# Kernel optimization log

Measured on AMD Instinct MI355X. Metric: run time of the kernel, lower is better.

The kernel has to match this reference:

```python
import jax, jax.numpy as jnp
import numpy as np

N_HEAD, D_K = 16, 64  # from init_kwargs (d_v == d_k)

def setup_inputs() -> dict:
    key = jax.random.key(0)
    ks = jax.random.split(key, 8)
    B, S, D, DFF = 8, 1024, 1024, 4096
    s = 1.0 / np.sqrt(D)
    return {
        "enc_input": jax.random.normal(ks[0], (B, S, D), jnp.float32),
        "mask": jnp.ones((B, 1, S), jnp.int32),
        "gap": 1,
        "wq": jax.random.normal(ks[1], (D, N_HEAD * D_K), jnp.float32) * s,
        "wk": jax.random.normal(ks[2], (D, N_HEAD * D_K), jnp.float32) * s,
        "wv": jax.random.normal(ks[3], (D, N_HEAD * D_K), jnp.float32) * s,
        "wo": jax.random.normal(ks[4], (N_HEAD * D_K, D), jnp.float32) * s,
        "w1": jax.random.normal(ks[5], (D, DFF), jnp.float32) * s,
        "b1": jnp.zeros((DFF,), jnp.float32),
        "w2": jax.random.normal(ks[6], (DFF, D), jnp.float32) * (1.0 / np.sqrt(DFF)),
        "b2": jnp.zeros((D,), jnp.float32),
    }

def reference(enc_input, mask, gap, wq, wk, wv, wo, w1, b1, w2, b2):
    # dropout=0, use_layer_norm=0, adapter=0 are hard-coded in EncoderLayer.__init__
    B, S, D = enc_input.shape
    H, dk = N_HEAD, D_K
    temperature = dk ** 0.5

    q = (enc_input @ wq).reshape(B, S, H, dk).transpose(0, 2, 1, 3)  # [B,H,S,dk]
    k = (enc_input @ wk).reshape(B, S, H, dk).transpose(0, 2, 1, 3)
    v = (enc_input @ wv).reshape(B, S, H, dk).transpose(0, 2, 1, 3)

    attn = jnp.einsum('bhqd,bhkd->bhqk', q / temperature, k)  # [B,H,S,S]
    # mask [B,1,S] -> unsqueeze head dim -> [B,1,1,S]
    attn = jnp.where(mask[:, None] == 0, jnp.float32(-1e9), attn)
    attn = jax.nn.softmax(attn, axis=-1)

    ctx = jnp.einsum('bhqk,bhkd->bhqd', attn, v)          # [B,H,S,dk]
    ctx = ctx.transpose(0, 2, 1, 3).reshape(B, S, H * dk)  # [B,S,D]
    enc = ctx @ wo + enc_input                              # attn residual

    ffn = jax.nn.relu(enc @ w1 + b1) @ w2 + b2
    out = ffn + enc                                         # ffn residual
    return out, attn
```

## Files before the change

kernel.cpp:

```cpp
#include <hip/hip_runtime.h>
#include <hip/hip_bf16.h>
#include <stdint.h>

typedef __bf16 bf16x8 __attribute__((ext_vector_type(8)));
typedef float  f32x4  __attribute__((ext_vector_type(4)));

typedef __attribute__((address_space(1))) void gvoid;
typedef __attribute__((address_space(3))) void lvoid;

__device__ __forceinline__ void async16(void* lds, const void* g) {
    __builtin_amdgcn_global_load_lds((gvoid*)g, (lvoid*)lds, 16, 0, 0);
}

__global__ void cvt_f32_to_bf16(const float* __restrict__ in,
                                __hip_bfloat16* __restrict__ out, long n) {
    long i = ((long)blockIdx.x * blockDim.x + threadIdx.x) * 4;
    if (i < n) {
        float4 v = *(const float4*)(in + i);
        __hip_bfloat162* d = (__hip_bfloat162*)(out + i);
        d[0] = __float22bfloat162_rn(make_float2(v.x, v.y));
        d[1] = __float22bfloat162_rn(make_float2(v.z, v.w));
    }
}

__global__ void transpose_f32_bf16(const float* __restrict__ in,
                                   __hip_bfloat16* __restrict__ out,
                                   int R, int C) {
    __shared__ float t[32][33];
    int c0 = blockIdx.x * 32, r0 = blockIdx.y * 32;
    int tx = threadIdx.x, ty = threadIdx.y;
#pragma unroll
    for (int i = 0; i < 4; ++i) {
        int r = r0 + ty + i * 8;
        t[ty + i * 8][tx] = in[(long)r * C + c0 + tx];
    }
    __syncthreads();
#pragma unroll
    for (int i = 0; i < 4; ++i) {
        int c = c0 + ty + i * 8;
        out[(long)c * R + r0 + tx] = __float2bfloat16(t[tx][ty + i * 8]);
    }
}

__global__ void transpose_v(const __hip_bfloat16* __restrict__ QKV,
                            __hip_bfloat16* __restrict__ Vt) {
    __shared__ __hip_bfloat16 t[32][33];
    int s0 = blockIdx.x * 32, d0 = blockIdx.y * 32, z = blockIdx.z;
    int b = z >> 4, h = z & 15;
    int tx = threadIdx.x, ty = threadIdx.y;
#pragma unroll
    for (int i = 0; i < 4; ++i) {
        int s = s0 + ty + i * 8;
        t[ty + i * 8][tx] = QKV[((long)b * 1024 + s) * 3072 + 2048 + h * 64 + d0 + tx];
    }
    __syncthreads();
#pragma unroll
    for (int i = 0; i < 4; ++i) {
        int d = d0 + ty + i * 8;
        Vt[((long)z * 64 + d) * 1024 + s0 + tx] = t[tx][ty + i * 8];
    }
}

__global__ void __launch_bounds__(256, 2)
attn_fused(const __hip_bfloat16* __restrict__ QKV,
           const __hip_bfloat16* __restrict__ Vt,
           const int* __restrict__ mask,
           float* __restrict__ attn,
           __hip_bfloat16* __restrict__ Ctx) {
    __shared__ __align__(16) __hip_bfloat16 sK[128 * 64];
    __shared__ __align__(16) __hip_bfloat16 sV[64 * 128];
    __shared__ __align__(16) __hip_bfloat16 sP[128 * 128];
    __shared__ float smadd[1024];

    const int tid = threadIdx.x, lane = tid & 63, wave = tid >> 6;
    const int r16 = lane & 15, kg = lane >> 4;

    const int dd = blockIdx.x;
    const int wgt = (dd & 7) * 128 + (dd >> 3);
    const int xblk = wgt & 7, z = wgt >> 3;
    const int b = z >> 4, h = z & 15;
    const int row0 = xblk * 128;
    const int wrow = wave * 32;

    const __hip_bfloat16* Qz = QKV + ((long)b * 1024 + row0) * 3072 + h * 64;
    const __hip_bfloat16* Kz = QKV + (long)b * 1024 * 3072 + 1024 + h * 64;
    const __hip_bfloat16* Vz = Vt + (long)z * 64 * 1024;
    float* attnZ = attn + (long)z * 1024 * 1024 + (long)row0 * 1024;

    for (int i = tid; i < 1024; i += 256)
        smadd[i] = mask[b * 1024 + i] ? 0.f : -1e9f;

    bf16x8 qa[2][2];
#pragma unroll
    for (int m = 0; m < 2; ++m)
#pragma unroll
        for (int kf = 0; kf < 2; ++kf)
            qa[m][kf] = *(const bf16x8*)(Qz + (long)(wrow + m * 16 + r16) * 3072 + kf * 32 + kg * 8);

    float mrow[2][4], lrow[2][4];
#pragma unroll
    for (int m = 0; m < 2; ++m)
#pragma unroll
        for (int i = 0; i < 4; ++i) { mrow[m][i] = -3e38f; lrow[m][i] = 0.f; }

    __syncthreads();

    const int ssw = (r16 & 7) << 4;

    for (int ct = 0; ct < 8; ++ct) {
#pragma unroll
        for (int j = 0; j < 4; ++j) {
            int c = wave * 4 + j;
            int s = c * 8 + (lane >> 3);
            int cb = (lane & 7) * 16;
            async16((char*)sK + c * 1024,
                    (const char*)(Kz + (long)(ct * 128 + s) * 3072) + (cb ^ ((s & 7) << 4)));
        }
        __syncthreads();

        f32x4 sacc[2][8];
#pragma unroll
        for (int m = 0; m < 2; ++m)
#pragma unroll
            for (int nf = 0; nf < 8; ++nf) sacc[m][nf] = f32x4{0.f, 0.f, 0.f, 0.f};

#pragma unroll
        for (int nf = 0; nf < 8; ++nf) {
            const char* kr = (const char*)sK + (nf * 16 + r16) * 128;
            bf16x8 bv0 = *(const bf16x8*)(kr + ((kg * 16) ^ ssw));
            bf16x8 bv1 = *(const bf16x8*)(kr + ((64 + kg * 16) ^ ssw));
#pragma unroll
            for (int m = 0; m < 2; ++m) {
                sacc[m][nf] = __builtin_amdgcn_mfma_f32_16x16x32_bf16(qa[m][0], bv0, sacc[m][nf], 0, 0, 0);
                sacc[m][nf] = __builtin_amdgcn_mfma_f32_16x16x32_bf16(qa[m][1], bv1, sacc[m][nf], 0, 0, 0);
            }
        }

        float madd[8];
#pragma unroll
        for (int nf = 0; nf < 8; ++nf) madd[nf] = smadd[ct * 128 + nf * 16 + r16];

#pragma unroll
        for (int m = 0; m < 2; ++m)
#pragma unroll
            for (int i = 0; i < 4; ++i) {
                float v[8];
                float tmax = -3e38f;
#pragma unroll
                for (int nf = 0; nf < 8; ++nf) {
                    float a = sacc[m][nf][i] * 0.125f + madd[nf];
                    v[nf] = a;
                    tmax = fmaxf(tmax, a);
                }
#pragma unroll
                for (int o = 1; o < 16; o <<= 1) tmax = fmaxf(tmax, __shfl_xor(tmax, o));
                float mnew = fmaxf(mrow[m][i], tmax);
                float corr = __expf(mrow[m][i] - mnew);
                float ts = 0.f;
#pragma unroll
                for (int nf = 0; nf < 8; ++nf) ts += __expf(v[nf] - mnew);
#pragma unroll
                for (int o = 1; o < 16; o <<= 1) ts += __shfl_xor(ts, o);
                lrow[m][i] = lrow[m][i] * corr + ts;
                mrow[m][i] = mnew;
            }
        __syncthreads();
    }

    float rinv[2][4];
#pragma unroll
    for (int m = 0; m < 2; ++m)
#pragma unroll
        for (int i = 0; i < 4; ++i) rinv[m][i] = 1.0f / lrow[m][i];

    f32x4 oacc[2][4];
#pragma unroll
    for (int m = 0; m < 2; ++m)
#pragma unroll
        for (int nf = 0; nf < 4; ++nf) oacc[m][nf] = f32x4{0.f, 0.f, 0.f, 0.f};

    for (int ct = 0; ct < 8; ++ct) {
#pragma unroll
        for (int j = 0; j < 4; ++j) {
            int c = wave * 4 + j;
            {
                int s = c * 8 + (lane >> 3);
                int cb = (lane & 7) * 16;
                async16((char*)sK + c * 1024,
                        (const char*)(Kz + (long)(ct * 128 + s) * 3072) + (cb ^ ((s & 7) << 4)));
            }
            {
                int dv = c * 4 + (lane >> 4);
                int cb = (lane & 15) * 16;
                async16((char*)sV + c * 1024,
                        (const char*)(Vz + (long)dv * 1024 + ct * 128) + (cb ^ ((dv & 7) << 4)));
            }
        }
        __syncthreads();

        f32x4 sacc[2][8];
#pragma unroll
        for (int m = 0; m < 2; ++m)
#pragma unroll
            for (int nf = 0; nf < 8; ++nf) sacc[m][nf] = f32x4{0.f, 0.f, 0.f, 0.f};

#pragma unroll
        for (int nf = 0; nf < 8; ++nf) {
            const char* kr = (const char*)sK + (nf * 16 + r16) * 128;
            bf16x8 bv0 = *(const bf16x8*)(kr + ((kg * 16) ^ ssw));
            bf16x8 bv1 = *(const bf16x8*)(kr + ((64 + kg * 16) ^ ssw));
#pragma unroll
            for (int m = 0; m < 2; ++m) {
                sacc[m][nf] = __builtin_amdgcn_mfma_f32_16x16x32_bf16(qa[m][0], bv0, sacc[m][nf], 0, 0, 0);
                sacc[m][nf] = __builtin_amdgcn_mfma_f32_16x16x32_bf16(qa[m][1], bv1, sacc[m][nf], 0, 0, 0);
            }
        }

        float madd[8];
#pragma unroll
        for (int nf = 0; nf < 8; ++nf) madd[nf] = smadd[ct * 128 + nf * 16 + r16];

#pragma unroll
        for (int m = 0; m < 2; ++m)
#pragma unroll
            for (int nf = 0; nf < 8; ++nf) {
                int scol = nf * 16 + r16;
#pragma unroll
                for (int i = 0; i < 4; ++i) {
                    int q = wrow + m * 16 + kg * 4 + i;
                    float p = __expf(sacc[m][nf][i] * 0.125f + madd[nf] - mrow[m][i]) * rinv[m][i];
                    attnZ[(long)q * 1024 + ct * 128 + scol] = p;
                    *(__hip_bfloat16*)((char*)sP + q * 256 + ((scol * 2) ^ ((q & 7) << 4))) =
                        __float2bfloat16(p);
                }
            }

#pragma unroll
        for (int ks = 0; ks < 4; ++ks) {
            bf16x8 pa[2], vv[4];
#pragma unroll
            for (int m = 0; m < 2; ++m)
                pa[m] = *(const bf16x8*)((const char*)sP + (wrow + m * 16 + r16) * 256 +
                                         ((ks * 64 + kg * 16) ^ ssw));
#pragma unroll
            for (int nf = 0; nf < 4; ++nf)
                vv[nf] = *(const bf16x8*)((const char*)sV + (nf * 16 + r16) * 256 +
                                          ((ks * 64 + kg * 16) ^ ssw));
#pragma unroll
            for (int m = 0; m < 2; ++m)
#pragma unroll
                for (int nf = 0; nf < 4; ++nf)
                    oacc[m][nf] = __builtin_amdgcn_mfma_f32_16x16x32_bf16(pa[m], vv[nf], oacc[m][nf], 0, 0, 0);
        }
        __syncthreads();
    }

#pragma unroll
    for (int m = 0; m < 2; ++m)
#pragma unroll
        for (int nf = 0; nf < 4; ++nf)
#pragma unroll
            for (int i = 0; i < 4; ++i) {
                int q = wrow + m * 16 + kg * 4 + i;
                Ctx[((long)b * 1024 + row0 + q) * 1024 + h * 64 + nf * 16 + r16] =
                    __float2bfloat16(oacc[m][nf][i]);
            }
}

template <int BM, int BN>
__global__ void __launch_bounds__(256)
gemm_bt(const __hip_bfloat16* __restrict__ Ab_, int lda,
        const __hip_bfloat16* __restrict__ Bt, int ldb,
        int K, float scale,
        const float* __restrict__ bias,
        const float* __restrict__ res, int ldres,
        float* __restrict__ Cf, __hip_bfloat16* __restrict__ Cb,
        int ldc, int relu) {
    constexpr int FM = BM / 32, FN = BN / 32;
    __shared__ __align__(16) __hip_bfloat16 sA[BM * 32];
    __shared__ __align__(16) __hip_bfloat16 sB[BN * 32];

    const int tid = threadIdx.x;
    const int lane = tid & 63, wave = tid >> 6;
    const int wr = wave >> 1, wc = wave & 1;
    const int r16 = lane & 15, kg = lane >> 4;
    const long row0 = (long)blockIdx.x * BM;
    const long col0 = (long)blockIdx.y * BN;

    const __hip_bfloat16* Ab = Ab_;
    const __hip_bfloat16* Bb = Bt;

    f32x4 acc[FM][FN] = {};

    for (int kt = 0; kt < K; kt += 32) {
        {
            constexpr int CHA = BM / 16;
            for (int c = wave; c < CHA; c += 4) {
                int e = c * 512 + lane * 8;
                int r = e >> 5, kk = e & 31;
                async16(&sA[c * 512], Ab + (row0 + r) * (long)lda + kt + kk);
            }
        }
        {
            constexpr int CHB = BN / 16;
            for (int c = wave; c < CHB; c += 4) {
                int e = c * 512 + lane * 8;
                int r = e >> 5, kk = e & 31;
                async16(&sB[c * 512], Bb + (col0 + r) * (long)ldb + kt + kk);
            }
        }
        __syncthreads();

        bf16x8 av[FM], bv[FN];
#pragma unroll
        for (int m = 0; m < FM; ++m)
            av[m] = *(const bf16x8*)&sA[(wr * (BM / 2) + m * 16 + r16) * 32 + kg * 8];
#pragma unroll
        for (int n = 0; n < FN; ++n)
            bv[n] = *(const bf16x8*)&sB[(wc * (BN / 2) + n * 16 + r16) * 32 + kg * 8];
#pragma unroll
        for (int m = 0; m < FM; ++m)
#pragma unroll
            for (int n = 0; n < FN; ++n)
                acc[m][n] = __builtin_amdgcn_mfma_f32_16x16x32_bf16(av[m], bv[n], acc[m][n], 0, 0, 0);
        __syncthreads();
    }

#pragma unroll
    for (int m = 0; m < FM; ++m) {
        const long rg0 = row0 + wr * (BM / 2) + m * 16 + kg * 4;
#pragma unroll
        for (int n = 0; n < FN; ++n) {
            const long cg = col0 + wc * (BN / 2) + n * 16 + r16;
#pragma unroll
            for (int i = 0; i < 4; ++i) {
                const long rg = rg0 + i;
                float v = acc[m][n][i] * scale;
                if (bias) v += bias[cg];
                if (relu) v = fmaxf(v, 0.f);
                if (res) v += res[rg * (long)ldres + cg];
                const long off = rg * (long)ldc + cg;
                if (Cf) Cf[off] = v;
                if (Cb) Cb[off] = __float2bfloat16(v);
            }
        }
    }
}

#define RDA(BUF, PM, ML, KS) \
    (*(const bf16x8*)(aRd + (BUF)*32768 + (PM)*16384 + (ML)*2048 + ((((KS)*64) + kg*16) ^ sw)))
#define RDB(BUF, PN, NL, KS) \
    (*(const bf16x8*)(bRd + (BUF)*32768 + (PN)*16384 + (NL)*2048 + ((((KS)*64) + kg*16) ^ sw)))
#define LOAD_A(BUF, PM)                          \
    _Pragma("unroll") for (int ml = 0; ml < 4; ++ml) \
    _Pragma("unroll") for (int ks = 0; ks < 2; ++ks) \
        a[ml][ks] = RDA(BUF, PM, ml, ks)
#define LOAD_B(DST, BUF, PN)                     \
    _Pragma("unroll") for (int nl = 0; nl < 2; ++nl) \
    _Pragma("unroll") for (int ks = 0; ks < 2; ++ks) \
        DST[nl][ks] = RDB(BUF, PN, nl, ks)
#define MFMA16(PM, PN, BB)                                                   \
    __builtin_amdgcn_s_setprio(1);                                           \
    _Pragma("unroll") for (int ks = 0; ks < 2; ++ks)                         \
    _Pragma("unroll") for (int ml = 0; ml < 4; ++ml)                         \
    _Pragma("unroll") for (int nl = 0; nl < 2; ++nl)                         \
        acc[(PM)*4 + ml][(PN)*2 + nl] = __builtin_amdgcn_mfma_f32_16x16x32_bf16( \
            a[ml][ks], BB[nl][ks], acc[(PM)*4 + ml][(PN)*2 + nl], 0, 0, 0);  \
    __builtin_amdgcn_s_setprio(0)
#define BAR asm volatile("s_barrier" ::: "memory")

__global__ void __launch_bounds__(512, 2)
gemm256(const __hip_bfloat16* __restrict__ A, int lda,
        const __hip_bfloat16* __restrict__ Bt, int ldb,
        int K, int Mtiles,
        const float* __restrict__ bias, int relu,
        __hip_bfloat16* __restrict__ C, int ldc) {
    __shared__ __align__(16) char lds[131072];
    const int NT = K >> 6;
    const int tid = threadIdx.x, lane = tid & 63, wave = tid >> 6;
    const int r16 = lane & 15, kg = lane >> 4;
    const int wr = wave >> 2, wc = wave & 3;
    const int sw = (r16 & 7) << 4;

    const int nwg = gridDim.x;
    const int q8 = nwg >> 3, r8 = nwg & 7;
    const int xcd = blockIdx.x & 7, rest = blockIdx.x >> 3;
    const int wg = (xcd < r8 ? xcd * (q8 + 1) : r8 * (q8 + 1) + (xcd - r8) * q8) + rest;
    const int tm = wg % Mtiles, tn = wg / Mtiles;
    const long row0 = (long)tm * 256, col0 = (long)tn * 256;

    const int idx = tid >> 3;
    const int slotp = ((tid & 7) ^ (idx & 7)) * 8;
    const __hip_bfloat16* aSrc[4];
    const __hip_bfloat16* bSrc[4];
#pragma unroll
    for (int j = 0; j < 4; ++j) {
        long ar = row0 + (j & 1) * 128 + (j >> 1) * 64 + idx;
        aSrc[j] = A + ar * lda + slotp;
        long br = col0 + ((j & 1) * 2 + (tid >> 8)) * 64 + (j >> 1) * 32 + (idx & 31);
        bSrc[j] = Bt + br * ldb + slotp;
    }

    char* ldsA = lds;
    char* ldsB = lds + 65536;
    const int stDst = wave * 1024;
    auto stA = [&](int v, int j) {
        async16(ldsA + ((v & 1) << 15) + (j << 13) + stDst, aSrc[j] + (v << 6));
    };
    auto stB = [&](int v, int j) {
        async16(ldsB + ((v & 1) << 15) + (j << 13) + stDst, bSrc[j] + (v << 6));
    };

    stA(0, 0); stA(0, 1); stB(0, 0); stB(0, 1);
    stA(0, 2); stA(0, 3); stB(0, 2); stB(0, 3);
    stA(1, 0); stA(1, 1); stB(1, 0); stB(1, 1);
    asm volatile("s_waitcnt vmcnt(4)" ::: "memory");
    BAR;

    f32x4 acc[8][4] = {};
    const char* aRd = ldsA + wr * 8192 + r16 * 128;
    const char* bRd = ldsB + wc * 4096 + r16 * 128;

    for (int u = 0; u < NT; u += 2) {
        const bool more = (u + 2) < NT;
        bf16x8 a[4][2], b0[2][2], b1[2][2];

        LOAD_A(0, 0);
        LOAD_B(b0, 0, 0);
        stA(u + 1, 2); stA(u + 1, 3);
        MFMA16(0, 0, b0);
        BAR;
        LOAD_B(b1, 0, 1);
        stB(u + 1, 2); stB(u + 1, 3);
        MFMA16(0, 1, b1);
        BAR;
        LOAD_A(0, 1);
        if (more) { stA(u + 2, 0); stA(u + 2, 1); }
        MFMA16(1, 0, b0);
        BAR;
        if (more) {
            stB(u + 2, 0); stB(u + 2, 1);
            asm volatile("s_waitcnt vmcnt(4)" ::: "memory");
        } else {
            asm volatile("s_waitcnt vmcnt(0)" ::: "memory");
        }
        MFMA16(1, 1, b1);
        BAR;
        LOAD_A(1, 0);
        LOAD_B(b0, 1, 0);
        if (more) { stA(u + 2, 2); stA(u + 2, 3); }
        MFMA16(0, 0, b0);
        BAR;
        LOAD_B(b1, 1, 1);
        if (more) { stB(u + 2, 2); stB(u + 2, 3); }
        MFMA16(0, 1, b1);
        BAR;
        LOAD_A(1, 1);
        if (more) { stA(u + 3, 0); stA(u + 3, 1); }
        MFMA16(1, 0, b0);
        BAR;
        if (more) {
            stB(u + 3, 0); stB(u + 3, 1);
            asm volatile("s_waitcnt vmcnt(4)" ::: "memory");
        }
        MFMA16(1, 1, b1);
        BAR;
    }

    const long crow = row0 + wr * 128, ccol = col0 + wc * 64;
#pragma unroll
    for (int mf = 0; mf < 8; ++mf)
#pragma unroll
        for (int nf = 0; nf < 4; ++nf) {
            const long col = ccol + nf * 16 + r16;
            const float bs = bias ? bias[col] : 0.f;
#pragma unroll
            for (int i = 0; i < 4; ++i) {
                const long row = crow + mf * 16 + kg * 4 + i;
                float v = acc[mf][nf][i] + bs;
                if (relu) v = fmaxf(v, 0.f);
                C[row * (long)ldc + col] = __float2bfloat16(v);
            }
        }
}

extern "C" void kernel_launch(void* const* d_in, const int* in_sizes, int n_in,
                              void* d_out, int out_size, void* d_ws, size_t ws_size,
                              hipStream_t stream) {
    const int B = 8, S = 1024, D = 1024, DFF = 4096;
    const long SD = (long)B * S * D;

    const float* X  = (const float*)d_in[0];
    const int*  msk = (const int*)d_in[1];
    const float* wq = (const float*)d_in[3];
    const float* wk = (const float*)d_in[4];
    const float* wv = (const float*)d_in[5];
    const float* wo = (const float*)d_in[6];
    const float* w1 = (const float*)d_in[7];
    const float* b1 = (const float*)d_in[8];
    const float* w2 = (const float*)d_in[9];
    const float* b2 = (const float*)d_in[10];

    float* out  = (float*)d_out;
    float* attn = out + SD;

    char* ws = (char*)d_ws;
    auto alloc = [&](size_t bytes) {
        char* p = ws;
        ws += (bytes + 255) & ~(size_t)255;
        return p;
    };
    __hip_bfloat16* Xb   = (__hip_bfloat16*)alloc(SD * 2);
    __hip_bfloat16* QKVb = (__hip_bfloat16*)alloc(SD * 3 * 2);
    __hip_bfloat16* Vt   = (__hip_bfloat16*)alloc(SD * 2);
    __hip_bfloat16* Ctx  = (__hip_bfloat16*)alloc(SD * 2);
    __hip_bfloat16* EncB = (__hip_bfloat16*)alloc(SD * 2);
    __hip_bfloat16* Hb   = (__hip_bfloat16*)alloc((long)B * S * DFF * 2);
    float*          EncF = (float*)alloc(SD * 4);
    __hip_bfloat16* Wcat = (__hip_bfloat16*)alloc((long)3 * D * D * 2);
    __hip_bfloat16* Wot  = (__hip_bfloat16*)alloc((long)D * D * 2);
    __hip_bfloat16* W1t  = (__hip_bfloat16*)alloc((long)D * DFF * 2);
    __hip_bfloat16* W2t  = (__hip_bfloat16*)alloc((long)D * DFF * 2);
    (void)ws_size; (void)in_sizes; (void)n_in; (void)out_size;

    dim3 tb(32, 8);
    cvt_f32_to_bf16<<<(int)(SD / 4 / 256), 256, 0, stream>>>(X, Xb, SD);
    transpose_f32_bf16<<<dim3(32, 32), tb, 0, stream>>>(wq, Wcat, D, D);
    transpose_f32_bf16<<<dim3(32, 32), tb, 0, stream>>>(wk, Wcat + (long)D * D, D, D);
    transpose_f32_bf16<<<dim3(32, 32), tb, 0, stream>>>(wv, Wcat + (long)2 * D * D, D, D);
    transpose_f32_bf16<<<dim3(32, 32), tb, 0, stream>>>(wo, Wot, D, D);
    transpose_f32_bf16<<<dim3(128, 32), tb, 0, stream>>>(w1, W1t, D, DFF);
    transpose_f32_bf16<<<dim3(32, 128), tb, 0, stream>>>(w2, W2t, DFF, D);

    gemm256<<<dim3(32 * 12), 512, 0, stream>>>(
        Xb, D, Wcat, D, D, 32, nullptr, 0, QKVb, 3 * D);

    transpose_v<<<dim3(32, 2, 128), tb, 0, stream>>>(QKVb, Vt);

    attn_fused<<<dim3(1024), 256, 0, stream>>>(QKVb, Vt, msk, attn, Ctx);

    gemm_bt<128, 128><<<dim3(64, 8), 256, 0, stream>>>(
        Ctx, D, Wot, D, D, 1.f,
        nullptr, X, D,
        EncF, EncB, D, 0);

    gemm256<<<dim3(32 * 16), 512, 0, stream>>>(
        EncB, D, W1t, D, D, 32, b1, 1, Hb, DFF);

    gemm_bt<128, 128><<<dim3(64, 8), 256, 0, stream>>>(
        Hb, DFF, W2t, DFF, DFF, 1.f,
        b2, EncF, D,
        out, nullptr, D, 0);
}
```

Before: 610.9 us.

## Split attention into stats and PV kernels with prefetched K/V tiles

The fused attention kernel is split in two. A lighter attn_stats kernel computes the row max and inverse sum at higher occupancy, double-buffering the K tiles. The attn_pv kernel reads those stats and overlaps staging of the next K/V tile with the softmax and PV work by holding the V fragments in registers. The fp32 intermediate after the attention residual is dropped, so the FFN residual is read from the bf16 EncB buffer. This cuts memory traffic but adds bf16 rounding to the residual path, and adds a kernel launch plus a small stats buffer round-trip.

```diff
diff --git a/kernel.cpp b/kernel.cpp
--- a/kernel.cpp
+++ b/kernel.cpp
@@ -61,15 +61,11 @@
     }
 }
 
-__global__ void __launch_bounds__(256, 2)
-attn_fused(const __hip_bfloat16* __restrict__ QKV,
-           const __hip_bfloat16* __restrict__ Vt,
+__global__ void __launch_bounds__(256, 4)
+attn_stats(const __hip_bfloat16* __restrict__ QKV,
            const int* __restrict__ mask,
-           float* __restrict__ attn,
-           __hip_bfloat16* __restrict__ Ctx) {
-    __shared__ __align__(16) __hip_bfloat16 sK[128 * 64];
-    __shared__ __align__(16) __hip_bfloat16 sV[64 * 128];
-    __shared__ __align__(16) __hip_bfloat16 sP[128 * 128];
+           float2* __restrict__ ML) {
+    __shared__ __align__(16) __hip_bfloat16 sK[2][128 * 64];
     __shared__ float smadd[1024];
 
     const int tid = threadIdx.x, lane = tid & 63, wave = tid >> 6;
@@ -84,8 +80,6 @@
 
     const __hip_bfloat16* Qz = QKV + ((long)b * 1024 + row0) * 3072 + h * 64;
     const __hip_bfloat16* Kz = QKV + (long)b * 1024 * 3072 + 1024 + h * 64;
-    const __hip_bfloat16* Vz = Vt + (long)z * 64 * 1024;
-    float* attnZ = attn + (long)z * 1024 * 1024 + (long)row0 * 1024;
 
     for (int i = tid; i < 1024; i += 256)
         smadd[i] = mask[b * 1024 + i] ? 0.f : -1e9f;
@@ -97,89 +91,144 @@
         for (int kf = 0; kf < 2; ++kf)
             qa[m][kf] = *(const bf16x8*)(Qz + (long)(wrow + m * 16 + r16) * 3072 + kf * 32 + kg * 8);
 
-    float mrow[2][4], lrow[2][4];
-#pragma unroll
-    for (int m = 0; m < 2; ++m)
-#pragma unroll
-        for (int i = 0; i < 4; ++i) { mrow[m][i] = -3e38f; lrow[m][i] = 0.f; }
-
-    __syncthreads();
-
-    const int ssw = (r16 & 7) << 4;
-
-    for (int ct = 0; ct < 8; ++ct) {
+    auto stageK = [&](int buf, int ct) {
 #pragma unroll
         for (int j = 0; j < 4; ++j) {
             int c = wave * 4 + j;
             int s = c * 8 + (lane >> 3);
             int cb = (lane & 7) * 16;
-            async16((char*)sK + c * 1024,
+            async16((char*)sK[buf] + c * 1024,
                     (const char*)(Kz + (long)(ct * 128 + s) * 3072) + (cb ^ ((s & 7) << 4)));
         }
+    };
+    stageK(0, 0);
+
+    float mrow[2][4], lrow[2][4];
+#pragma unroll
+    for (int m = 0; m < 2; ++m)
+#pragma unroll
+        for (int i = 0; i < 4; ++i) { mrow[m][i] = -3e38f; lrow[m][i] = 0.f; }
+
+    const int ssw = (r16 & 7) << 4;
+
+    for (int ct = 0; ct < 8; ++ct) {
+        asm volatile("s_waitcnt vmcnt(0)" ::: "memory");
         __syncthreads();
-
-        f32x4 sacc[2][8];
+        if (ct < 7) stageK((ct + 1) & 1, ct + 1);
+        const char* base = (const char*)sK[ct & 1];
+
+#pragma unroll
+        for (int g = 0; g < 2; ++g) {
+            f32x4 sacc[2][4];
+#pragma unroll
+            for (int m = 0; m < 2; ++m)
+#pragma unroll
+                for (int nf = 0; nf < 4; ++nf) sacc[m][nf] = f32x4{0.f, 0.f, 0.f, 0.f};
+
+#pragma unroll
+            for (int nf = 0; nf < 4; ++nf) {
+                const char* kr = base + ((g * 4 + nf) * 16 + r16) * 128;
+                bf16x8 bv0 = *(const bf16x8*)(kr + ((kg * 16) ^ ssw));
+                bf16x8 bv1 = *(const bf16x8*)(kr + ((64 + kg * 16) ^ ssw));
+#pragma unroll
+                for (int m = 0; m < 2; ++m) {
+                    sacc[m][nf] = __builtin_amdgcn_mfma_f32_16x16x32_bf16(qa[m][0], bv0, sacc[m][nf], 0, 0, 0);
+                    sacc[m][nf] = __builtin_amdgcn_mfma_f32_16x16x32_bf16(qa[m][1], bv1, sacc[m][nf], 0, 0, 0);
+                }
+            }
+
+            float madd[4];
+#pragma unroll
+            for (int nf = 0; nf < 4; ++nf) madd[nf] = smadd[ct * 128 + (g * 4 + nf) * 16 + r16];
+
+#pragma unroll
+            for (int m = 0; m < 2; ++m)
+#pragma unroll
+                for (int i = 0; i < 4; ++i) {
+                    float v[4];
+                    float tmax = -3e38f;
+#pragma unroll
+                    for (int nf = 0; nf < 4; ++nf) {
+                        float a = sacc[m][nf][i] * 0.125f + madd[nf];
+                        v[nf] = a;
+                        tmax = fmaxf(tmax, a);
+                    }
+#pragma unroll
+                    for (int o = 1; o < 16; o <<= 1) tmax = fmaxf(tmax, __shfl_xor(tmax, o));
+                    float mnew = fmaxf(mrow[m][i], tmax);
+                    float corr = __expf(mrow[m][i] - mnew);
+                    float ts = 0.f;
+#pragma unroll
+                    for (int nf = 0; nf < 4; ++nf) ts += __expf(v[nf] - mnew);
+#pragma unroll
+                    for (int o = 1; o < 16; o <<= 1) ts += __shfl_xor(ts, o);
+                    lrow[m][i] = lrow[m][i] * corr + ts;
+                    mrow[m][i] = mnew;
+                }
+        }
+    }
+
+    if (r16 == 0) {
+        float2* mlz = ML + (long)z * 1024 + row0;
 #pragma unroll
         for (int m = 0; m < 2; ++m)
 #pragma unroll
-            for (int nf = 0; nf < 8; ++nf) sacc[m][nf] = f32x4{0.f, 0.f, 0.f, 0.f};
-
-#pragma unroll
-        for (int nf = 0; nf < 8; ++nf) {
-            const char* kr = (const char*)sK + (nf * 16 + r16) * 128;
-            bf16x8 bv0 = *(const bf16x8*)(kr + ((kg * 16) ^ ssw));
-            bf16x8 bv1 = *(const bf16x8*)(kr + ((64 + kg * 16) ^ ssw));
-#pragma unroll
-            for (int m = 0; m < 2; ++m) {
-                sacc[m][nf] = __builtin_amdgcn_mfma_f32_16x16x32_bf16(qa[m][0], bv0, sacc[m][nf], 0, 0, 0);
-                sacc[m][nf] = __builtin_amdgcn_mfma_f32_16x16x32_bf16(qa[m][1], bv1, sacc[m][nf], 0, 0, 0);
-            }
-        }
-
-        float madd[8];
-#pragma unroll
-        for (int nf = 0; nf < 8; ++nf) madd[nf] = smadd[ct * 128 + nf * 16 + r16];
-
+            for (int i = 0; i < 4; ++i)
+                mlz[wrow + m * 16 + kg * 4 + i] = make_float2(mrow[m][i], 1.f / lrow[m][i]);
+    }
+}
+
+__global__ void __launch_bounds__(256, 2)
+attn_pv(const __hip_bfloat16* __restrict__ QKV,
+        const __hip_bfloat16* __restrict__ Vt,
+        const float2* __restrict__ ML,
+        const int* __restrict__ mask,
+        float* __restrict__ attn,
+        __hip_bfloat16* __restrict__ Ctx) {
+    __shared__ __align__(16) __hip_bfloat16 sK[128 * 64];
+    __shared__ __align__(16) __hip_bfloat16 sV[64 * 128];
+    __shared__ __align__(16) __hip_bfloat16 sP[128 * 128];
+    __shared__ float smadd[1024];
+
+    const int tid = threadIdx.x, lane = tid & 63, wave = tid >> 6;
+    const int r16 = lane & 15, kg = lane >> 4;
+
+    const int dd = blockIdx.x;
+    const int wgt = (dd & 7) * 128 + (dd >> 3);
+    const int xblk = wgt & 7, z = wgt >> 3;
+    const int b = z >> 4, h = z & 15;
+    const int row0 = xblk * 128;
+    const int wrow = wave * 32;
+
+    const __hip_bfloat16* Qz = QKV + ((long)b * 1024 + row0) * 3072 + h * 64;
+    const __hip_bfloat16* Kz = QKV + (long)b * 1024 * 3072 + 1024 + h * 64;
+    const __hip_bfloat16* Vz = Vt + (long)z * 64 * 1024;
+    float* attnZ = attn + (long)z * 1024 * 1024 + (long)row0 * 1024;
+
+    for (int i = tid; i < 1024; i += 256)
+        smadd[i] = mask[b * 1024 + i] ? 0.f : -1e9f;
+
+    bf16x8 qa[2][2];
+#pragma unroll
+    for (int m = 0; m < 2; ++m)
+#pragma unroll
+        for (int kf = 0; kf < 2; ++kf)
+            qa[m][kf] = *(const bf16x8*)(Qz + (long)(wrow + m * 16 + r16) * 3072 + kf * 32 + kg * 8);
+
+    float mrow[2][4], rinv[2][4];
+    {
+        const float2* mlz = ML + (long)z * 1024 + row0;
 #pragma unroll
         for (int m = 0; m < 2; ++m)
 #pragma unroll
             for (int i = 0; i < 4; ++i) {
-                float v[8];
-                float tmax = -3e38f;
-#pragma unroll
-                for (int nf = 0; nf < 8; ++nf) {
-                    float a = sacc[m][nf][i] * 0.125f + madd[nf];
-                    v[nf] = a;
-                    tmax = fmaxf(tmax, a);
-                }
-#pragma unroll
-                for (int o = 1; o < 16; o <<= 1) tmax = fmaxf(tmax, __shfl_xor(tmax, o));
-                float mnew = fmaxf(mrow[m][i], tmax);
-                float corr = __expf(mrow[m][i] - mnew);
-                float ts = 0.f;
-#pragma unroll
-                for (int nf = 0; nf < 8; ++nf) ts += __expf(v[nf] - mnew);
-#pragma unroll
-                for (int o = 1; o < 16; o <<= 1) ts += __shfl_xor(ts, o);
-                lrow[m][i] = lrow[m][i] * corr + ts;
-                mrow[m][i] = mnew;
-            }
-        __syncthreads();
-    }
-
-    float rinv[2][4];
-#pragma unroll
-    for (int m = 0; m < 2; ++m)
-#pragma unroll
-        for (int i = 0; i < 4; ++i) rinv[m][i] = 1.0f / lrow[m][i];
-
-    f32x4 oacc[2][4];
-#pragma unroll
-    for (int m = 0; m < 2; ++m)
-#pragma unroll
-        for (int nf = 0; nf < 4; ++nf) oacc[m][nf] = f32x4{0.f, 0.f, 0.f, 0.f};
-
-    for (int ct = 0; ct < 8; ++ct) {
+                float2 t = mlz[wrow + m * 16 + kg * 4 + i];
+                mrow[m][i] = t.x;
+                rinv[m][i] = t.y;
+            }
+    }
+
+    auto stageKV = [&](int ct) {
 #pragma unroll
         for (int j = 0; j < 4; ++j) {
             int c = wave * 4 + j;
@@ -196,6 +245,19 @@
                         (const char*)(Vz + (long)dv * 1024 + ct * 128) + (cb ^ ((dv & 7) << 4)));
             }
         }
+    };
+    stageKV(0);
+
+    f32x4 oacc[2][4];
+#pragma unroll
+    for (int m = 0; m < 2; ++m)
+#pragma unroll
+        for (int nf = 0; nf < 4; ++nf) oacc[m][nf] = f32x4{0.f, 0.f, 0.f, 0.f};
+
+    const int ssw = (r16 & 7) << 4;
+
+    for (int ct = 0; ct < 8; ++ct) {
+        asm volatile("s_waitcnt vmcnt(0)" ::: "memory");
         __syncthreads();
 
         f32x4 sacc[2][8];
@@ -215,6 +277,17 @@
                 sacc[m][nf] = __builtin_amdgcn_mfma_f32_16x16x32_bf16(qa[m][1], bv1, sacc[m][nf], 0, 0, 0);
             }
         }
+
+        bf16x8 vv[4][4];
+#pragma unroll
+        for (int ks = 0; ks < 4; ++ks)
+#pragma unroll
+            for (int nf = 0; nf < 4; ++nf)
+                vv[ks][nf] = *(const bf16x8*)((const char*)sV + (nf * 16 + r16) * 256 +
+                                              ((ks * 64 + kg * 16) ^ ssw));
+
+        __syncthreads();
+        if (ct < 7) stageKV(ct + 1);
 
         float madd[8];
 #pragma unroll
@@ -237,22 +310,17 @@
 
 #pragma unroll
         for (int ks = 0; ks < 4; ++ks) {
-            bf16x8 pa[2], vv[4];
+            bf16x8 pa[2];
 #pragma unroll
             for (int m = 0; m < 2; ++m)
                 pa[m] = *(const bf16x8*)((const char*)sP + (wrow + m * 16 + r16) * 256 +
                                          ((ks * 64 + kg * 16) ^ ssw));
 #pragma unroll
-            for (int nf = 0; nf < 4; ++nf)
-                vv[nf] = *(const bf16x8*)((const char*)sV + (nf * 16 + r16) * 256 +
-                                          ((ks * 64 + kg * 16) ^ ssw));
-#pragma unroll
             for (int m = 0; m < 2; ++m)
 #pragma unroll
                 for (int nf = 0; nf < 4; ++nf)
-                    oacc[m][nf] = __builtin_amdgcn_mfma_f32_16x16x32_bf16(pa[m], vv[nf], oacc[m][nf], 0, 0, 0);
-        }
-        __syncthreads();
+                    oacc[m][nf] = __builtin_amdgcn_mfma_f32_16x16x32_bf16(pa[m], vv[ks][nf], oacc[m][nf], 0, 0, 0);
+        }
     }
 
 #pragma unroll
@@ -269,11 +337,12 @@
 
 template <int BM, int BN>
 __global__ void __launch_bounds__(256)
-gemm_bt(const __hip_bfloat16* __restrict__ Ab_, int lda,
+gemm_bt(const __hip_bfloat16* __restrict__ Ab, int lda,
         const __hip_bfloat16* __restrict__ Bt, int ldb,
-        int K, float scale,
+        int K,
         const float* __restrict__ bias,
-        const float* __restrict__ res, int ldres,
+        const float* __restrict__ resf,
+        const __hip_bfloat16* __restrict__ resb, int ldres,
         float* __restrict__ Cf, __hip_bfloat16* __restrict__ Cb,
         int ldc, int relu) {
     constexpr int FM = BM / 32, FN = BN / 32;
@@ -286,9 +355,6 @@
     const int r16 = lane & 15, kg = lane >> 4;
     const long row0 = (long)blockIdx.x * BM;
     const long col0 = (long)blockIdx.y * BN;
-
-    const __hip_bfloat16* Ab = Ab_;
-    const __hip_bfloat16* Bb = Bt;
 
     f32x4 acc[FM][FN] = {};
 
@@ -306,7 +372,7 @@
             for (int c = wave; c < CHB; c += 4) {
                 int e = c * 512 + lane * 8;
                 int r = e >> 5, kk = e & 31;
-                async16(&sB[c * 512], Bb + (col0 + r) * (long)ldb + kt + kk);
+                async16(&sB[c * 512], Bt + (col0 + r) * (long)ldb + kt + kk);
             }
         }
         __syncthreads();
@@ -335,10 +401,11 @@
 #pragma unroll
             for (int i = 0; i < 4; ++i) {
                 const long rg = rg0 + i;
-                float v = acc[m][n][i] * scale;
+                float v = acc[m][n][i];
                 if (bias) v += bias[cg];
                 if (relu) v = fmaxf(v, 0.f);
-                if (res) v += res[rg * (long)ldres + cg];
+                if (resf) v += resf[rg * (long)ldres + cg];
+                if (resb) v += __bfloat162float(resb[rg * (long)ldres + cg]);
                 const long off = rg * (long)ldc + cg;
                 if (Cf) Cf[off] = v;
                 if (Cb) Cb[off] = __float2bfloat16(v);
@@ -430,14 +497,17 @@
         stA(u + 1, 2); stA(u + 1, 3);
         MFMA16(0, 0, b0);
         BAR;
+
         LOAD_B(b1, 0, 1);
         stB(u + 1, 2); stB(u + 1, 3);
         MFMA16(0, 1, b1);
         BAR;
+
         LOAD_A(0, 1);
         if (more) { stA(u + 2, 0); stA(u + 2, 1); }
         MFMA16(1, 0, b0);
         BAR;
+
         if (more) {
             stB(u + 2, 0); stB(u + 2, 1);
             asm volatile("s_waitcnt vmcnt(4)" ::: "memory");
@@ -446,19 +516,23 @@
         }
         MFMA16(1, 1, b1);
         BAR;
+
         LOAD_A(1, 0);
         LOAD_B(b0, 1, 0);
         if (more) { stA(u + 2, 2); stA(u + 2, 3); }
         MFMA16(0, 0, b0);
         BAR;
+
         LOAD_B(b1, 1, 1);
         if (more) { stB(u + 2, 2); stB(u + 2, 3); }
         MFMA16(0, 1, b1);
         BAR;
+
         LOAD_A(1, 1);
         if (more) { stA(u + 3, 0); stA(u + 3, 1); }
         MFMA16(1, 0, b0);
         BAR;
+
         if (more) {
             stB(u + 3, 0); stB(u + 3, 1);
             asm volatile("s_waitcnt vmcnt(4)" ::: "memory");
@@ -516,7 +590,7 @@
     __hip_bfloat16* Ctx  = (__hip_bfloat16*)alloc(SD * 2);
     __hip_bfloat16* EncB = (__hip_bfloat16*)alloc(SD * 2);
     __hip_bfloat16* Hb   = (__hip_bfloat16*)alloc((long)B * S * DFF * 2);
-    float*          EncF = (float*)alloc(SD * 4);
+    float2*         ML   = (float2*)alloc((long)128 * 1024 * sizeof(float2));
     __hip_bfloat16* Wcat = (__hip_bfloat16*)alloc((long)3 * D * D * 2);
     __hip_bfloat16* Wot  = (__hip_bfloat16*)alloc((long)D * D * 2);
     __hip_bfloat16* W1t  = (__hip_bfloat16*)alloc((long)D * DFF * 2);
@@ -537,18 +611,19 @@
 
     transpose_v<<<dim3(32, 2, 128), tb, 0, stream>>>(QKVb, Vt);
 
-    attn_fused<<<dim3(1024), 256, 0, stream>>>(QKVb, Vt, msk, attn, Ctx);
+    attn_stats<<<dim3(1024), 256, 0, stream>>>(QKVb, msk, ML);
+    attn_pv<<<dim3(1024), 256, 0, stream>>>(QKVb, Vt, ML, msk, attn, Ctx);
 
     gemm_bt<128, 128><<<dim3(64, 8), 256, 0, stream>>>(
-        Ctx, D, Wot, D, D, 1.f,
-        nullptr, X, D,
-        EncF, EncB, D, 0);
+        Ctx, D, Wot, D, D,
+        nullptr, X, nullptr, D,
+        nullptr, EncB, D, 0);
 
     gemm256<<<dim3(32 * 16), 512, 0, stream>>>(
         EncB, D, W1t, D, D, 32, b1, 1, Hb, DFF);
 
     gemm_bt<128, 128><<<dim3(64, 8), 256, 0, stream>>>(
-        Hb, DFF, W2t, DFF, DFF, 1.f,
-        b2, EncF, D,
+        Hb, DFF, W2t, DFF, DFF,
+        b2, nullptr, EncB, D,
         out, nullptr, D, 0);
 }
```

New measurement: 762.5 us. +24.8%, slower.
